# Kernel tuning notes

Hardware: AMD Instinct MI355X
Metric: run time of the kernel (lower is better)

## Reference

```python
import jax, jax.numpy as jnp
import numpy as np

N_HEADS = 32
N_KV_HEADS = 8
HEAD_DIM = 64
DIM = 2048
MAX_CTX = 2048
N_REP = N_HEADS // N_KV_HEADS


def setup_inputs() -> dict:
    key = jax.random.key(0)
    ks = jax.random.split(key, 8)
    B, S = 1, 2048
    x = jax.random.normal(ks[0], (B, S, DIM), dtype=jnp.float32)
    # RoPE frequencies (real cos/sin, [S, head_dim//2])
    inv_freq = 1.0 / (10000.0 ** (np.arange(0, HEAD_DIM, 2, dtype=np.float32) / HEAD_DIM))
    t = np.arange(S, dtype=np.float32)
    freqs = np.outer(t, inv_freq)  # [S, HEAD_DIM//2]
    freqs_cos = jnp.asarray(np.cos(freqs), dtype=jnp.float32)
    freqs_sin = jnp.asarray(np.sin(freqs), dtype=jnp.float32)
    input_pos = jnp.arange(S, dtype=jnp.int32)
    scale = 0.02
    wq = jax.random.normal(ks[1], (N_HEADS * HEAD_DIM, DIM), dtype=jnp.float32) * scale
    wk = jax.random.normal(ks[2], (N_KV_HEADS * HEAD_DIM, DIM), dtype=jnp.float32) * scale
    wv = jax.random.normal(ks[3], (N_KV_HEADS * HEAD_DIM, DIM), dtype=jnp.float32) * scale
    wo = jax.random.normal(ks[4], (DIM, N_HEADS * HEAD_DIM), dtype=jnp.float32) * scale
    k_cache = jnp.zeros((B, N_KV_HEADS, MAX_CTX, HEAD_DIM), dtype=jnp.float32)
    v_cache = jnp.zeros((B, N_KV_HEADS, MAX_CTX, HEAD_DIM), dtype=jnp.float32)
    return {"x": x, "freqs_cos": freqs_cos, "freqs_sin": freqs_sin,
            "input_pos": input_pos, "wq": wq, "wk": wk, "wv": wv, "wo": wo,
            "k_cache": k_cache, "v_cache": v_cache}


def _apply_rope(x, cos, sin):
    # x: [B, S, H, HEAD_DIM]; cos/sin: [S, HEAD_DIM//2]
    xr = x[..., 0::2]
    xi = x[..., 1::2]
    c = cos[None, :, None, :]
    s = sin[None, :, None, :]
    out_r = xr * c - xi * s
    out_i = xr * s + xi * c
    # interleave back: stack on new trailing axis then flatten pairs
    out = jnp.stack([out_r, out_i], axis=-1)
    return out.reshape(x.shape)


def reference(x, freqs_cos, freqs_sin, input_pos, wq, wk, wv, wo, k_cache, v_cache):
    B, S, _ = x.shape
    q = (x @ wq.T).reshape(B, S, N_HEADS, HEAD_DIM)
    k = (x @ wk.T).reshape(B, S, N_KV_HEADS, HEAD_DIM)
    v = (x @ wv.T).reshape(B, S, N_KV_HEADS, HEAD_DIM)
    q = _apply_rope(q, freqs_cos, freqs_sin)
    k = _apply_rope(k, freqs_cos, freqs_sin)
    q = q.transpose(0, 2, 1, 3)   # [B, H, S, D]
    k = k.transpose(0, 2, 1, 3)   # [B, KV, S, D]
    v = v.transpose(0, 2, 1, 3)
    # KV-cache scatter update at input_pos
    k_full = k_cache.at[:, :, input_pos].set(k)   # [B, KV, MAX_CTX, D]
    v_full = v_cache.at[:, :, input_pos].set(v)
    # causal mask rows gathered at input_pos: [S, MAX_CTX]
    causal = jnp.tril(jnp.ones((MAX_CTX, MAX_CTX), dtype=bool))
    attn_mask = causal[input_pos]
    # GQA repeat_interleave along head dim
    k_rep = jnp.repeat(k_full, N_REP, axis=1)    # [B, H, MAX_CTX, D]
    v_rep = jnp.repeat(v_full, N_REP, axis=1)
    scale = 1.0 / jnp.sqrt(jnp.asarray(HEAD_DIM, dtype=x.dtype))
    scores = jnp.einsum('bhsd,bhtd->bhst', q, k_rep) * scale  # [B, H, S, MAX_CTX]
    neg = jnp.asarray(jnp.finfo(scores.dtype).min, dtype=scores.dtype)
    scores = jnp.where(attn_mask[None, None, :, :], scores, neg)
    attn = jax.nn.softmax(scores, axis=-1)
    y = jnp.einsum('bhst,bhtd->bhsd', attn, v_rep)  # [B, H, S, D]
    y = y.transpose(0, 2, 1, 3).reshape(B, S, N_HEADS * HEAD_DIM)
    return y @ wo.T
```

## Files before the change

kernel.cpp:

```cpp
#include <hip/hip_runtime.h>


typedef __attribute__((ext_vector_type(8))) __bf16 bf16x8;
typedef __attribute__((ext_vector_type(4))) float f32x4;

#define S_LEN 2048
#define DIMN  2048
#define NH    32
#define NKV   8
#define HD    64
#define QKVF  3072

struct DoPair { static constexpr bool value = true; };
struct OnlyB  { static constexpr bool value = false; };

__device__ __forceinline__ ushort f2bf(float f) {
  union { float f; unsigned u; } v; v.f = f;
  unsigned r = v.u + 0x7fffu + ((v.u >> 16) & 1u);
  return (ushort)(r >> 16);
}
__device__ __forceinline__ unsigned pack_bf2_rz(float a, float b) {
  union { float f; unsigned u; } va, vb; va.f = a; vb.f = b;
  return (va.u >> 16) | (vb.u & 0xffff0000u);
}
__device__ __forceinline__ float bf2f(ushort u) {
  union { unsigned u; float f; } v; v.u = ((unsigned)u) << 16;
  return v.f;
}
__device__ __forceinline__ void gld_lds16(const void* g, void* l) {
  __builtin_amdgcn_global_load_lds(
      (const __attribute__((address_space(1))) unsigned int*)g,
      (__attribute__((address_space(3))) unsigned int*)l, 16, 0, 0);
}

__global__ __launch_bounds__(256) void convert_all(
    const float* __restrict__ x, const float* __restrict__ wq,
    const float* __restrict__ wk, const float* __restrict__ wv,
    const float* __restrict__ wo, ushort* __restrict__ xb,
    ushort* __restrict__ wqkvb, ushort* __restrict__ wob) {
  const size_t NX = 4u * 1024 * 1024;
  const size_t NK = 1024 * 1024;
  size_t idx = ((size_t)blockIdx.x * 256 + threadIdx.x) * 4;
  const float* src; ushort* dst;
  if (idx < NX)                { src = x  + idx;                  dst = xb + idx; }
  else if (idx < 2 * NX)       { src = wq + (idx - NX);           dst = wqkvb + (idx - NX); }
  else if (idx < 2 * NX + NK)  { src = wk + (idx - 2 * NX);       dst = wqkvb + NX + (idx - 2 * NX); }
  else if (idx < 2 * NX + 2*NK){ src = wv + (idx - 2 * NX - NK);  dst = wqkvb + NX + NK + (idx - 2 * NX - NK); }
  else                         { src = wo + (idx - 2 * NX - 2*NK);dst = wob + (idx - 2 * NX - 2 * NK); }
  float4 v = *(const float4*)src;
  ushort4 o; o.x = f2bf(v.x); o.y = f2bf(v.y); o.z = f2bf(v.z); o.w = f2bf(v.w);
  *(ushort4*)dst = o;
}

template <int OUT_BF16, int BM, int BN>
__global__ __launch_bounds__(256) void gemm_bt(
    const ushort* __restrict__ A, const ushort* __restrict__ B,
    void* __restrict__ Cv, int M, int N, int K) {
  constexpr int IB = BM / 32;
  constexpr int JB = BN / 32;
  constexpr int NGA = BM / 8;
  constexpr int GPW = (BM + BN) / 32;
  __shared__ __align__(16) ushort As[2][BM * 64];
  __shared__ __align__(16) ushort Bs[2][BN * 64];
  const int n0 = blockIdx.x * BN, m0 = blockIdx.y * BM;
  const int t = threadIdx.x;
  const int lane = t & 63, wave = t >> 6;
  const int wm = (wave >> 1) * (BM / 2), wn = (wave & 1) * (BN / 2);
  const int col = lane & 15, quad = lane >> 4;
  const int sw = col & 7;
  const int lrow = lane >> 3;
  const int scol = ((lane & 7) ^ lrow) * 8;
  f32x4 acc[IB][JB] = {};

  auto stage = [&](int b, int kk) {
#pragma unroll
    for (int c = 0; c < GPW; ++c) {
      int g = wave * GPW + c;
      if (g < NGA)
        gld_lds16(&A[(size_t)(m0 + g * 8 + lrow) * K + kk + scol], &As[b][g * 8 * 64]);
      else
        gld_lds16(&B[(size_t)(n0 + (g - NGA) * 8 + lrow) * K + kk + scol],
                  &Bs[b][(g - NGA) * 8 * 64]);
    }
  };

  stage(0, 0);
  __syncthreads();
  for (int kk = 0; kk < K; kk += 64) {
    const int b = (kk >> 6) & 1;
    if (kk + 64 < K) stage(b ^ 1, kk + 64);
#pragma unroll
    for (int c = 0; c < 2; ++c) {
      const int chs = ((c * 4 + quad) ^ sw) * 8;
      bf16x8 af[IB], bfr[JB];
#pragma unroll
      for (int i = 0; i < IB; ++i)
        af[i] = *(const bf16x8*)&As[b][(wm + i * 16 + col) * 64 + chs];
#pragma unroll
      for (int j = 0; j < JB; ++j)
        bfr[j] = *(const bf16x8*)&Bs[b][(wn + j * 16 + col) * 64 + chs];
#pragma unroll
      for (int i = 0; i < IB; ++i)
#pragma unroll
        for (int j = 0; j < JB; ++j)
          acc[i][j] = __builtin_amdgcn_mfma_f32_16x16x32_bf16(af[i], bfr[j], acc[i][j], 0, 0, 0);
    }
    __syncthreads();
  }
#pragma unroll
  for (int i = 0; i < IB; ++i)
#pragma unroll
    for (int r = 0; r < 4; ++r) {
      int m = m0 + wm + i * 16 + quad * 4 + r;
      if (OUT_BF16) {
        ushort* C = (ushort*)Cv;
#pragma unroll
        for (int j = 0; j < JB; ++j)
          C[(size_t)m * N + n0 + wn + j * 16 + col] = f2bf(acc[i][j][r]);
      } else {
        float* C = (float*)Cv;
#pragma unroll
        for (int j = 0; j < JB; ++j)
          C[(size_t)m * N + n0 + wn + j * 16 + col] = acc[i][j][r];
      }
    }
}

__global__ __launch_bounds__(256) void rope_layout(
    const ushort* __restrict__ qkv, const float* __restrict__ fc,
    const float* __restrict__ fs, ushort* __restrict__ qb,
    ushort* __restrict__ kb, ushort* __restrict__ vt) {
  __shared__ ushort T[64][72];
  const int hh = blockIdx.x;
  const int s0 = blockIdx.y * 256;
  const int t = threadIdx.x;
  if (hh < 32) {
    ushort* dst = qb + (size_t)hh * S_LEN * 64;
    const float qs = 0.18033688011112042f;
    const int sr = t >> 4, dc = (t & 15) * 4, i0 = (t & 15) * 2;
#pragma unroll 4
    for (int pass = 0; pass < 16; ++pass) {
      int s = s0 + pass * 16 + sr;
      ushort4 vv = *(const ushort4*)&qkv[(size_t)s * QKVF + hh * 64 + dc];
      float2 cc = *(const float2*)&fc[s * 32 + i0];
      float2 ss = *(const float2*)&fs[s * 32 + i0];
      float xr0 = bf2f(vv.x), xi0 = bf2f(vv.y), xr1 = bf2f(vv.z), xi1 = bf2f(vv.w);
      ushort4 ov;
      ov.x = f2bf((xr0 * cc.x - xi0 * ss.x) * qs); ov.y = f2bf((xr0 * ss.x + xi0 * cc.x) * qs);
      ov.z = f2bf((xr1 * cc.y - xi1 * ss.y) * qs); ov.w = f2bf((xr1 * ss.y + xi1 * cc.y) * qs);
      *(ushort4*)&dst[(size_t)s * 64 + dc] = ov;
    }
  } else if (hh < 40) {
    const int kh2 = hh - 32;
    const int sr8 = t >> 3;
    const int ch = t & 7;
#pragma unroll 2
    for (int pass = 0; pass < 8; ++pass) {
      int s = s0 + pass * 32 + sr8;
      ushort in[8], out[8];
      *(int4*)&in[0] = *(const int4*)&qkv[(size_t)s * QKVF + 2048 + kh2 * 64 + ch * 8];
      float4 cc = *(const float4*)&fc[s * 32 + ch * 4];
      float4 ss4 = *(const float4*)&fs[s * 32 + ch * 4];
      const float* cp = &cc.x; const float* sp = &ss4.x;
#pragma unroll
      for (int i = 0; i < 4; ++i) {
        float xr = bf2f(in[2 * i]), xi = bf2f(in[2 * i + 1]);
        out[2 * i]     = f2bf(xr * cp[i] - xi * sp[i]);
        out[2 * i + 1] = f2bf(xr * sp[i] + xi * cp[i]);
      }
      int r = s & 63, tile = s >> 6;
      size_t pos = ((size_t)(kh2 * 32 + tile)) * 4096 +
                   ((size_t)(((ch >> 2) * 4 + (r >> 4)) * 64 + (ch & 3) * 16 + (r & 15))) * 8;
      *(int4*)&kb[pos] = *(const int4*)&out[0];
    }
  } else {
    const int vh = hh - 40;
    for (int sub = 0; sub < 4; ++sub) {
      int sb = s0 + sub * 64;
      int sr = t >> 2, dc = (t & 3) * 16;
      ushort tmp[16];
      *(int4*)&tmp[0] = *(const int4*)&qkv[(size_t)(sb + sr) * QKVF + 2560 + vh * 64 + dc];
      *(int4*)&tmp[8] = *(const int4*)&qkv[(size_t)(sb + sr) * QKVF + 2560 + vh * 64 + dc + 8];
      __syncthreads();
      const int pcol = ((sr & 15) << 2) | (sr >> 4);
#pragma unroll
      for (int k = 0; k < 16; ++k) T[dc + k][pcol] = tmp[k];
      __syncthreads();
      int d = t >> 2;
      int ch0 = (t & 3) * 2, ch1 = ch0 + 1;
      int tile = sb >> 6;
      size_t base = ((size_t)(vh * 32 + tile)) * 4096;
      size_t p0 = base + ((size_t)(((ch0 >> 2) * 4 + (d >> 4)) * 64 + (ch0 & 3) * 16 + (d & 15))) * 8;
      size_t p1 = base + ((size_t)(((ch1 >> 2) * 4 + (d >> 4)) * 64 + (ch1 & 3) * 16 + (d & 15))) * 8;
      *(int4*)&vt[p0] = *(const int4*)&T[d][ch0 * 8];
      *(int4*)&vt[p1] = *(const int4*)&T[d][ch1 * 8];
    }
  }
}

__global__ __launch_bounds__(256, 2) void attn(
    const ushort* __restrict__ qbg, const ushort* __restrict__ kbg,
    const ushort* __restrict__ vtg, ushort* __restrict__ yb) {
  __shared__ __align__(16) ushort Ps[4][2][16][64];
  const int kvh = blockIdx.x;
  const int y = blockIdx.y;
  const int sA = y, sB = 127 - y;
  const int ntA = (sA >> 2) + 1;
  const int ntB = (sB >> 2) + 1;
  const int wave = threadIdx.x >> 6;
  const int lane = threadIdx.x & 63;
  const int col = lane & 15, quad = lane >> 4;
  const int h = kvh * 4 + wave;
  const ushort* qh = qbg + (size_t)h * S_LEN * HD;
  const ushort* kbase = kbg + (size_t)kvh * 32 * 4096;
  const ushort* vbase = vtg + (size_t)kvh * 32 * 4096;

  const int q0A = sA * 16, q0B = sB * 16;
  bf16x8 qfA[2], qfB[2];
  qfA[0] = *(const bf16x8*)&qh[(size_t)(q0A + col) * HD + quad * 8];
  qfA[1] = *(const bf16x8*)&qh[(size_t)(q0A + col) * HD + 32 + quad * 8];
  qfB[0] = *(const bf16x8*)&qh[(size_t)(q0B + col) * HD + quad * 8];
  qfB[1] = *(const bf16x8*)&qh[(size_t)(q0B + col) * HD + 32 + quad * 8];
  float lA[4] = {}, lB[4] = {};
  f32x4 oA[4] = {}, oB[4] = {};

  auto tile_body = [&](int t, bool maskA, bool maskB, auto tag) {
    constexpr bool DOA = decltype(tag)::value;
    const ushort* kt  = kbase + (size_t)t * 4096;
    const ushort* vtt = vbase + (size_t)t * 4096;
    f32x4 scA[4] = {}, scB[4] = {};
#pragma unroll
    for (int c = 0; c < 2; ++c) {
#pragma unroll
      for (int j = 0; j < 4; ++j) {
        bf16x8 kf = *(const bf16x8*)&kt[((c * 4 + j) * 64 + lane) * 8];
        scB[j] = __builtin_amdgcn_mfma_f32_16x16x32_bf16(qfB[c], kf, scB[j], 0, 0, 0);
        if constexpr (DOA)
          scA[j] = __builtin_amdgcn_mfma_f32_16x16x32_bf16(qfA[c], kf, scA[j], 0, 0, 0);
      }
    }
#pragma unroll
    for (int r = 0; r < 4; ++r) {
      const int prow = quad * 4 + r;
      const int psw = (((col >> 1) ^ (prow & 7)) << 3) + ((col & 1) << 2);
      {
        const int rowq = q0B + prow;
        float pr[4];
#pragma unroll
        for (int j = 0; j < 4; ++j) {
          float e = __builtin_amdgcn_exp2f(scB[j][r]);
          if (maskB) e = (t * 64 + j * 16 + col > rowq) ? 0.f : e;
          pr[j] = e;
        }
        lB[r] += (pr[0] + pr[1]) + (pr[2] + pr[3]);
        uint2 pk;
        pk.x = pack_bf2_rz(pr[0], pr[1]);
        pk.y = pack_bf2_rz(pr[2], pr[3]);
        *(uint2*)&Ps[wave][1][prow][psw] = pk;
      }
      if constexpr (DOA) {
        const int rowq = q0A + prow;
        float pr[4];
#pragma unroll
        for (int j = 0; j < 4; ++j) {
          float e = __builtin_amdgcn_exp2f(scA[j][r]);
          if (maskA) e = (t * 64 + j * 16 + col > rowq) ? 0.f : e;
          pr[j] = e;
        }
        lA[r] += (pr[0] + pr[1]) + (pr[2] + pr[3]);
        uint2 pk;
        pk.x = pack_bf2_rz(pr[0], pr[1]);
        pk.y = pack_bf2_rz(pr[2], pr[3]);
        *(uint2*)&Ps[wave][0][prow][psw] = pk;
      }
    }
#pragma unroll
    for (int c = 0; c < 2; ++c) {
      const int psr = ((c * 4 + quad) ^ (col & 7)) * 8;
      bf16x8 pfB = *(const bf16x8*)&Ps[wave][1][col][psr];
      bf16x8 pfA;
      if constexpr (DOA) pfA = *(const bf16x8*)&Ps[wave][0][col][psr];
#pragma unroll
      for (int db = 0; db < 4; ++db) {
        bf16x8 vf = *(const bf16x8*)&vtt[((c * 4 + db) * 64 + lane) * 8];
        oB[db] = __builtin_amdgcn_mfma_f32_16x16x32_bf16(pfB, vf, oB[db], 0, 0, 0);
        if constexpr (DOA)
          oA[db] = __builtin_amdgcn_mfma_f32_16x16x32_bf16(pfA, vf, oA[db], 0, 0, 0);
      }
    }
  };

  int t = 0;
  for (; t < ntA; ++t) tile_body(t, t == ntA - 1, false, DoPair{});
  for (; t < ntB - 1; ++t) tile_body(t, false, false, OnlyB{});
  tile_body(ntB - 1, false, true, OnlyB{});

  auto write_out = [&](const f32x4 (&o)[4], const float (&l)[4], int q0) {
#pragma unroll
    for (int r = 0; r < 4; ++r) {
      float ls = l[r];
      ls += __shfl_xor(ls, 1);
      ls += __shfl_xor(ls, 2);
      ls += __shfl_xor(ls, 4);
      ls += __shfl_xor(ls, 8);
      float inv = 1.0f / ls;
      int rowq = q0 + quad * 4 + r;
#pragma unroll
      for (int db = 0; db < 4; ++db)
        yb[(size_t)rowq * (NH * HD) + h * HD + db * 16 + col] = f2bf(o[db][r] * inv);
    }
  };
  write_out(oA, lA, q0A);
  write_out(oB, lB, q0B);
}

extern "C" void kernel_launch(void* const* d_in, const int* in_sizes, int n_in,
                              void* d_out, int out_size, void* d_ws, size_t ws_size,
                              hipStream_t stream) {
  (void)in_sizes; (void)n_in; (void)out_size; (void)ws_size;
  const float* x  = (const float*)d_in[0];
  const float* fc = (const float*)d_in[1];
  const float* fs = (const float*)d_in[2];
  const float* wq = (const float*)d_in[4];
  const float* wk = (const float*)d_in[5];
  const float* wv = (const float*)d_in[6];
  const float* wo = (const float*)d_in[7];
  ushort* w = (ushort*)d_ws;
  const size_t M1 = 1024 * 1024;
  ushort* xb    = w;
  ushort* wqkvb = w + 4 * M1;
  ushort* wob   = w + 10 * M1;
  ushort* qkvb  = w + 14 * M1;
  ushort* qb    = w + 20 * M1;
  ushort* kb    = w + 24 * M1;
  ushort* vt    = w + 25 * M1;
  ushort* yb    = w + 26 * M1;

  convert_all<<<14336, 256, 0, stream>>>(x, wq, wk, wv, wo, xb, wqkvb, wob);
  gemm_bt<1, 128, 96><<<dim3(QKVF / 96, S_LEN / 128), 256, 0, stream>>>(xb, wqkvb, qkvb, S_LEN, QKVF, DIMN);
  rope_layout<<<dim3(48, 8), 256, 0, stream>>>(qkvb, fc, fs, qb, kb, vt);
  attn<<<dim3(NKV, 64), 256, 0, stream>>>(qb, kb, vt, yb);
  gemm_bt<0, 64, 128><<<dim3(DIMN / 128, S_LEN / 64), 256, 0, stream>>>(yb, wob, d_out, S_LEN, DIMN, NH * HD);
}
```

Baseline: 211.8 us.

## Prefetch next K/V tile into registers with double-buffered attention loop

Restructures the attention tile loop so that the K and V fragments for tile t+1 are loaded from global memory into a second register set while tile t is computed. The loop alternates between the two buffers. Compile-time specialization of the paired and B-only paths is replaced by runtime branches. This is meant to hide global load latency behind MFMA and exp work, at the cost of 32 extra VGPR vectors, which may lower occupancy or cause spills. The runtime branches may also add overhead.

```diff
diff --git a/kernel.cpp b/kernel.cpp
--- a/kernel.cpp
+++ b/kernel.cpp
@@ -10,9 +10,6 @@
 #define NKV   8
 #define HD    64
 #define QKVF  3072
-
-struct DoPair { static constexpr bool value = true; };
-struct OnlyB  { static constexpr bool value = false; };
 
 __device__ __forceinline__ ushort f2bf(float f) {
   union { float f; unsigned u; } v; v.f = f;
@@ -224,41 +221,62 @@
   float lA[4] = {}, lB[4] = {};
   f32x4 oA[4] = {}, oB[4] = {};
 
-  auto tile_body = [&](int t, bool maskA, bool maskB, auto tag) {
-    constexpr bool DOA = decltype(tag)::value;
-    const ushort* kt  = kbase + (size_t)t * 4096;
+  bf16x8 k0[8], v0[8], k1[8], v1[8];
+
+  auto loadK = [&](bf16x8 (&kf)[8], int t) {
+    const ushort* kt = kbase + (size_t)t * 4096;
+#pragma unroll
+    for (int p = 0; p < 8; ++p) kf[p] = *(const bf16x8*)&kt[(p * 64 + lane) * 8];
+  };
+  auto loadV = [&](bf16x8 (&vf)[8], int t) {
     const ushort* vtt = vbase + (size_t)t * 4096;
+#pragma unroll
+    for (int p = 0; p < 8; ++p) vf[p] = *(const bf16x8*)&vtt[(p * 64 + lane) * 8];
+  };
+
+  auto body = [&](bf16x8 (&kfc)[8], bf16x8 (&vfc)[8],
+                  bf16x8 (&kfn)[8], bf16x8 (&vfn)[8], int t) {
+    const bool doA = (t < ntA);
+    const bool maskA = (t == ntA - 1);
+    const bool maskB = (t == ntB - 1);
+    const bool pre = (t + 1 < ntB);
+    if (pre) loadK(kfn, t + 1);
     f32x4 scA[4] = {}, scB[4] = {};
 #pragma unroll
-    for (int c = 0; c < 2; ++c) {
-#pragma unroll
-      for (int j = 0; j < 4; ++j) {
-        bf16x8 kf = *(const bf16x8*)&kt[((c * 4 + j) * 64 + lane) * 8];
-        scB[j] = __builtin_amdgcn_mfma_f32_16x16x32_bf16(qfB[c], kf, scB[j], 0, 0, 0);
-        if constexpr (DOA)
-          scA[j] = __builtin_amdgcn_mfma_f32_16x16x32_bf16(qfA[c], kf, scA[j], 0, 0, 0);
-      }
+    for (int c = 0; c < 2; ++c)
+#pragma unroll
+      for (int j = 0; j < 4; ++j)
+        scB[j] = __builtin_amdgcn_mfma_f32_16x16x32_bf16(qfB[c], kfc[c * 4 + j], scB[j], 0, 0, 0);
+    if (doA) {
+#pragma unroll
+      for (int c = 0; c < 2; ++c)
+#pragma unroll
+        for (int j = 0; j < 4; ++j)
+          scA[j] = __builtin_amdgcn_mfma_f32_16x16x32_bf16(qfA[c], kfc[c * 4 + j], scA[j], 0, 0, 0);
     }
 #pragma unroll
     for (int r = 0; r < 4; ++r) {
       const int prow = quad * 4 + r;
       const int psw = (((col >> 1) ^ (prow & 7)) << 3) + ((col & 1) << 2);
-      {
-        const int rowq = q0B + prow;
-        float pr[4];
-#pragma unroll
-        for (int j = 0; j < 4; ++j) {
-          float e = __builtin_amdgcn_exp2f(scB[j][r]);
-          if (maskB) e = (t * 64 + j * 16 + col > rowq) ? 0.f : e;
-          pr[j] = e;
-        }
-        lB[r] += (pr[0] + pr[1]) + (pr[2] + pr[3]);
-        uint2 pk;
-        pk.x = pack_bf2_rz(pr[0], pr[1]);
-        pk.y = pack_bf2_rz(pr[2], pr[3]);
-        *(uint2*)&Ps[wave][1][prow][psw] = pk;
-      }
-      if constexpr (DOA) {
+      const int rowq = q0B + prow;
+      float pr[4];
+#pragma unroll
+      for (int j = 0; j < 4; ++j) {
+        float e = __builtin_amdgcn_exp2f(scB[j][r]);
+        if (maskB) e = (t * 64 + j * 16 + col > rowq) ? 0.f : e;
+        pr[j] = e;
+      }
+      lB[r] += (pr[0] + pr[1]) + (pr[2] + pr[3]);
+      uint2 pk;
+      pk.x = pack_bf2_rz(pr[0], pr[1]);
+      pk.y = pack_bf2_rz(pr[2], pr[3]);
+      *(uint2*)&Ps[wave][1][prow][psw] = pk;
+    }
+    if (doA) {
+#pragma unroll
+      for (int r = 0; r < 4; ++r) {
+        const int prow = quad * 4 + r;
+        const int psw = (((col >> 1) ^ (prow & 7)) << 3) + ((col & 1) << 2);
         const int rowq = q0A + prow;
         float pr[4];
 #pragma unroll
@@ -274,26 +292,36 @@
         *(uint2*)&Ps[wave][0][prow][psw] = pk;
       }
     }
+    if (pre) loadV(vfn, t + 1);
 #pragma unroll
     for (int c = 0; c < 2; ++c) {
       const int psr = ((c * 4 + quad) ^ (col & 7)) * 8;
       bf16x8 pfB = *(const bf16x8*)&Ps[wave][1][col][psr];
-      bf16x8 pfA;
-      if constexpr (DOA) pfA = *(const bf16x8*)&Ps[wave][0][col][psr];
-#pragma unroll
-      for (int db = 0; db < 4; ++db) {
-        bf16x8 vf = *(const bf16x8*)&vtt[((c * 4 + db) * 64 + lane) * 8];
-        oB[db] = __builtin_amdgcn_mfma_f32_16x16x32_bf16(pfB, vf, oB[db], 0, 0, 0);
-        if constexpr (DOA)
-          oA[db] = __builtin_amdgcn_mfma_f32_16x16x32_bf16(pfA, vf, oA[db], 0, 0, 0);
-      }
-    }
-  };
-
-  int t = 0;
-  for (; t < ntA; ++t) tile_body(t, t == ntA - 1, false, DoPair{});
-  for (; t < ntB - 1; ++t) tile_body(t, false, false, OnlyB{});
-  tile_body(ntB - 1, false, true, OnlyB{});
+#pragma unroll
+      for (int db = 0; db < 4; ++db)
+        oB[db] = __builtin_amdgcn_mfma_f32_16x16x32_bf16(pfB, vfc[c * 4 + db], oB[db], 0, 0, 0);
+    }
+    if (doA) {
+#pragma unroll
+      for (int c = 0; c < 2; ++c) {
+        const int psr = ((c * 4 + quad) ^ (col & 7)) * 8;
+        bf16x8 pfA = *(const bf16x8*)&Ps[wave][0][col][psr];
+#pragma unroll
+        for (int db = 0; db < 4; ++db)
+          oA[db] = __builtin_amdgcn_mfma_f32_16x16x32_bf16(pfA, vfc[c * 4 + db], oA[db], 0, 0, 0);
+      }
+    }
+  };
+
+  loadK(k0, 0);
+  loadV(v0, 0);
+  for (int t = 0; t < ntB;) {
+    body(k0, v0, k1, v1, t);
+    ++t;
+    if (t >= ntB) break;
+    body(k1, v1, k0, v0, t);
+    ++t;
+  }
 
   auto write_out = [&](const f32x4 (&o)[4], const float (&l)[4], int q0) {
 #pragma unroll
```

Result: no change. 213.1 us (+0.6%).

## Split attention KV tiles across two waves per head and merge partial sums

Applied to the files above, without the earlier changes.

Each attention block now handles a single query head with two waves that take alternating KV tiles (split-K), instead of one block running four heads of a KV group with one wave each. The partial outputs and row sums from the second wave are merged through shared memory before the first wave normalizes and writes. This quadruples the block count to 2048 small blocks, shortening each wave's serial tile loop and raising parallelism. In exchange, K/V tiles are no longer shared across the four heads of a KV group within one block, and the merge adds a barrier plus shared-memory traffic.

```diff
diff --git a/kernel.cpp b/kernel.cpp
--- a/kernel.cpp
+++ b/kernel.cpp
@@ -198,19 +198,20 @@
   }
 }
 
-__global__ __launch_bounds__(256, 2) void attn(
+__global__ __launch_bounds__(128, 4) void attn(
     const ushort* __restrict__ qbg, const ushort* __restrict__ kbg,
     const ushort* __restrict__ vtg, ushort* __restrict__ yb) {
-  __shared__ __align__(16) ushort Ps[4][2][16][64];
-  const int kvh = blockIdx.x;
+  __shared__ __align__(16) ushort Ps[2][2][16][64];
+  __shared__ __align__(16) float Mrg[2][64][20];
+  const int h = blockIdx.x;
   const int y = blockIdx.y;
+  const int kvh = h >> 2;
+  const int khalf = threadIdx.x >> 6;
+  const int lane = threadIdx.x & 63;
+  const int col = lane & 15, quad = lane >> 4;
   const int sA = y, sB = 127 - y;
   const int ntA = (sA >> 2) + 1;
   const int ntB = (sB >> 2) + 1;
-  const int wave = threadIdx.x >> 6;
-  const int lane = threadIdx.x & 63;
-  const int col = lane & 15, quad = lane >> 4;
-  const int h = kvh * 4 + wave;
   const ushort* qh = qbg + (size_t)h * S_LEN * HD;
   const ushort* kbase = kbg + (size_t)kvh * 32 * 4096;
   const ushort* vbase = vtg + (size_t)kvh * 32 * 4096;
@@ -224,13 +225,15 @@
   float lA[4] = {}, lB[4] = {};
   f32x4 oA[4] = {}, oB[4] = {};
 
-  auto tile_body = [&](int t, bool maskA, bool maskB, auto tag) {
+  auto body = [&](int t, auto tag) {
     constexpr bool DOA = decltype(tag)::value;
     const ushort* kt  = kbase + (size_t)t * 4096;
     const ushort* vtt = vbase + (size_t)t * 4096;
+    const bool maskA = (t == ntA - 1);
+    const bool maskB = (t == ntB - 1);
     f32x4 scA[4] = {}, scB[4] = {};
 #pragma unroll
-    for (int c = 0; c < 2; ++c) {
+    for (int c = 0; c < 2; ++c)
 #pragma unroll
       for (int j = 0; j < 4; ++j) {
         bf16x8 kf = *(const bf16x8*)&kt[((c * 4 + j) * 64 + lane) * 8];
@@ -238,27 +241,29 @@
         if constexpr (DOA)
           scA[j] = __builtin_amdgcn_mfma_f32_16x16x32_bf16(qfA[c], kf, scA[j], 0, 0, 0);
       }
-    }
 #pragma unroll
     for (int r = 0; r < 4; ++r) {
       const int prow = quad * 4 + r;
       const int psw = (((col >> 1) ^ (prow & 7)) << 3) + ((col & 1) << 2);
-      {
-        const int rowq = q0B + prow;
-        float pr[4];
-#pragma unroll
-        for (int j = 0; j < 4; ++j) {
-          float e = __builtin_amdgcn_exp2f(scB[j][r]);
-          if (maskB) e = (t * 64 + j * 16 + col > rowq) ? 0.f : e;
-          pr[j] = e;
-        }
-        lB[r] += (pr[0] + pr[1]) + (pr[2] + pr[3]);
-        uint2 pk;
-        pk.x = pack_bf2_rz(pr[0], pr[1]);
-        pk.y = pack_bf2_rz(pr[2], pr[3]);
-        *(uint2*)&Ps[wave][1][prow][psw] = pk;
-      }
-      if constexpr (DOA) {
+      const int rowq = q0B + prow;
+      float pr[4];
+#pragma unroll
+      for (int j = 0; j < 4; ++j) {
+        float e = __builtin_amdgcn_exp2f(scB[j][r]);
+        if (maskB) e = (t * 64 + j * 16 + col > rowq) ? 0.f : e;
+        pr[j] = e;
+      }
+      lB[r] += (pr[0] + pr[1]) + (pr[2] + pr[3]);
+      uint2 pk;
+      pk.x = pack_bf2_rz(pr[0], pr[1]);
+      pk.y = pack_bf2_rz(pr[2], pr[3]);
+      *(uint2*)&Ps[khalf][1][prow][psw] = pk;
+    }
+    if constexpr (DOA) {
+#pragma unroll
+      for (int r = 0; r < 4; ++r) {
+        const int prow = quad * 4 + r;
+        const int psw = (((col >> 1) ^ (prow & 7)) << 3) + ((col & 1) << 2);
         const int rowq = q0A + prow;
         float pr[4];
 #pragma unroll
@@ -271,15 +276,15 @@
         uint2 pk;
         pk.x = pack_bf2_rz(pr[0], pr[1]);
         pk.y = pack_bf2_rz(pr[2], pr[3]);
-        *(uint2*)&Ps[wave][0][prow][psw] = pk;
+        *(uint2*)&Ps[khalf][0][prow][psw] = pk;
       }
     }
 #pragma unroll
     for (int c = 0; c < 2; ++c) {
       const int psr = ((c * 4 + quad) ^ (col & 7)) * 8;
-      bf16x8 pfB = *(const bf16x8*)&Ps[wave][1][col][psr];
+      bf16x8 pfB = *(const bf16x8*)&Ps[khalf][1][col][psr];
       bf16x8 pfA;
-      if constexpr (DOA) pfA = *(const bf16x8*)&Ps[wave][0][col][psr];
+      if constexpr (DOA) pfA = *(const bf16x8*)&Ps[khalf][0][col][psr];
 #pragma unroll
       for (int db = 0; db < 4; ++db) {
         bf16x8 vf = *(const bf16x8*)&vtt[((c * 4 + db) * 64 + lane) * 8];
@@ -290,28 +295,57 @@
     }
   };
 
-  int t = 0;
-  for (; t < ntA; ++t) tile_body(t, t == ntA - 1, false, DoPair{});
-  for (; t < ntB - 1; ++t) tile_body(t, false, false, OnlyB{});
-  tile_body(ntB - 1, false, true, OnlyB{});
-
-  auto write_out = [&](const f32x4 (&o)[4], const float (&l)[4], int q0) {
+  for (int t = khalf; t < ntB; t += 2) {
+    if (t < ntA) body(t, DoPair{});
+    else         body(t, OnlyB{});
+  }
+
+  if (khalf == 1) {
+#pragma unroll
+    for (int db = 0; db < 4; ++db)
+#pragma unroll
+      for (int r = 0; r < 4; ++r) {
+        Mrg[0][lane][db * 4 + r] = oA[db][r];
+        Mrg[1][lane][db * 4 + r] = oB[db][r];
+      }
 #pragma unroll
     for (int r = 0; r < 4; ++r) {
-      float ls = l[r];
-      ls += __shfl_xor(ls, 1);
-      ls += __shfl_xor(ls, 2);
-      ls += __shfl_xor(ls, 4);
-      ls += __shfl_xor(ls, 8);
-      float inv = 1.0f / ls;
-      int rowq = q0 + quad * 4 + r;
-#pragma unroll
-      for (int db = 0; db < 4; ++db)
-        yb[(size_t)rowq * (NH * HD) + h * HD + db * 16 + col] = f2bf(o[db][r] * inv);
-    }
-  };
-  write_out(oA, lA, q0A);
-  write_out(oB, lB, q0B);
+      Mrg[0][lane][16 + r] = lA[r];
+      Mrg[1][lane][16 + r] = lB[r];
+    }
+  }
+  __syncthreads();
+  if (khalf == 0) {
+#pragma unroll
+    for (int db = 0; db < 4; ++db)
+#pragma unroll
+      for (int r = 0; r < 4; ++r) {
+        oA[db][r] += Mrg[0][lane][db * 4 + r];
+        oB[db][r] += Mrg[1][lane][db * 4 + r];
+      }
+#pragma unroll
+    for (int r = 0; r < 4; ++r) {
+      lA[r] += Mrg[0][lane][16 + r];
+      lB[r] += Mrg[1][lane][16 + r];
+    }
+    auto write_out = [&](const f32x4 (&o)[4], const float (&l)[4], int q0) {
+#pragma unroll
+      for (int r = 0; r < 4; ++r) {
+        float ls = l[r];
+        ls += __shfl_xor(ls, 1);
+        ls += __shfl_xor(ls, 2);
+        ls += __shfl_xor(ls, 4);
+        ls += __shfl_xor(ls, 8);
+        float inv = 1.0f / ls;
+        int rowq = q0 + quad * 4 + r;
+#pragma unroll
+        for (int db = 0; db < 4; ++db)
+          yb[(size_t)rowq * (NH * HD) + h * HD + db * 16 + col] = f2bf(o[db][r] * inv);
+      }
+    };
+    write_out(oA, lA, q0A);
+    write_out(oB, lB, q0B);
+  }
 }
 
 extern "C" void kernel_launch(void* const* d_in, const int* in_sizes, int n_in,
@@ -339,6 +373,6 @@
   convert_all<<<14336, 256, 0, stream>>>(x, wq, wk, wv, wo, xb, wqkvb, wob);
   gemm_bt<1, 128, 96><<<dim3(QKVF / 96, S_LEN / 128), 256, 0, stream>>>(xb, wqkvb, qkvb, S_LEN, QKVF, DIMN);
   rope_layout<<<dim3(48, 8), 256, 0, stream>>>(qkvb, fc, fs, qb, kb, vt);
-  attn<<<dim3(NKV, 64), 256, 0, stream>>>(qb, kb, vt, yb);
+  attn<<<dim3(32, 64), 128, 0, stream>>>(qb, kb, vt, yb);
   gemm_bt<0, 64, 128><<<dim3(DIMN / 128, S_LEN / 64), 256, 0, stream>>>(yb, wob, d_out, S_LEN, DIMN, NH * HD);
 }
```

New measurement: 254.4 us. +20.1%, slower.
